# Kernel tuning notes

Hardware: AMD Instinct MI355X
Metric: run time of the kernel (lower is better)

Reference implementation:

```python
import jax, jax.numpy as jnp
import numpy as np

B, T, DM = 2, 2048, 2048
HQ, HKV, D = 16, 4, 128
MULT = 0.08838834764831845  # attn_output_multiplier = 1/sqrt(key_size)
ROPE_BASE = 10000.0


def rotate_half(x):
    x1, x2 = jnp.split(x, 2, axis=-1)
    return jnp.concatenate((-x2, x1), axis=-1)


def rope_tables(seq_len, dim, dtype):
    inv_freq = 1.0 / (ROPE_BASE ** (jnp.arange(0, dim, 2, dtype=jnp.float32) / dim))
    t = jnp.arange(seq_len, dtype=jnp.float32)
    freqs = jnp.outer(t, inv_freq)              # [T, D/2]
    emb = jnp.concatenate((freqs, freqs), axis=-1)  # [T, D]
    cos = jnp.cos(emb)[None, :, None, :].astype(dtype)  # [1, T, 1, D]
    sin = jnp.sin(emb)[None, :, None, :].astype(dtype)
    return cos, sin


def setup_inputs() -> dict:
    key = jax.random.key(0)
    ks = jax.random.split(key, 5)
    s = 1.0 / np.sqrt(DM)
    x = jax.random.normal(ks[0], (B, T, DM), dtype=jnp.float32)
    Wq = jax.random.normal(ks[1], (DM, HQ * D), dtype=jnp.float32) * s
    Wk = jax.random.normal(ks[2], (DM, HKV * D), dtype=jnp.float32) * s
    Wv = jax.random.normal(ks[3], (DM, HKV * D), dtype=jnp.float32) * s
    Wo = jax.random.normal(ks[4], (HQ * D, DM), dtype=jnp.float32) * s
    mask = jnp.tril(jnp.ones((T, T), dtype=bool))[None, None]  # [1,1,T,T] causal
    return {"x": x, "mask": mask, "Wq": Wq, "Wk": Wk, "Wv": Wv, "Wo": Wo}


def reference(x, mask, Wq, Wk, Wv, Wo):
    Bx, Tx, _ = x.shape
    q = (x @ Wq).reshape(Bx, Tx, HQ, D)
    k = (x @ Wk).reshape(Bx, Tx, HKV, D)
    v = (x @ Wv).reshape(Bx, Tx, HKV, D)
    cos, sin = rope_tables(Tx, D, x.dtype)
    q = q * cos + rotate_half(q) * sin
    k = k * cos + rotate_half(k) * sin
    n_rep = HQ // HKV
    k = jnp.repeat(k, n_rep, axis=2)  # [B,T,HQ,D] (repeat_interleave)
    v = jnp.repeat(v, n_rep, axis=2)
    logits = jnp.einsum('bqhd,bkhd->bhqk', q, k) * MULT
    logits = jnp.where(mask, logits, jnp.float32(-jnp.inf))
    attn = jax.nn.softmax(logits.astype(jnp.float32), axis=-1).astype(x.dtype)
    out = jnp.einsum('bhqk,bkhd->bqhd', attn, v).reshape(Bx, Tx, HQ * D)
    return out @ Wo
```

## Files before the change

### kernel.cpp

```cpp
#include <hip/hip_runtime.h>
#include <cstdint>
#include <cstddef>

#define T_SEQ 2048
#define DMODEL 2048
#define HQ 16
#define HKV 4
#define HD 128

typedef __attribute__((ext_vector_type(4))) float f32x4;
typedef __attribute__((ext_vector_type(8))) short bf16x8;
typedef __attribute__((ext_vector_type(4))) short short4v;
typedef __attribute__((ext_vector_type(2))) short short2v;
typedef __attribute__((ext_vector_type(4))) unsigned uint4v;

__device__ __forceinline__ short f2bf(float f) {
  unsigned u = __builtin_bit_cast(unsigned, f);
  u = (u + 0x7FFFu + ((u >> 16) & 1u)) >> 16;
  return (short)u;
}
__device__ __forceinline__ float bf2f(short s) {
  unsigned u = ((unsigned)(unsigned short)s) << 16;
  return __builtin_bit_cast(float, u);
}
__device__ __forceinline__ unsigned pk_hi16(float a, float b) {
  return __builtin_amdgcn_perm(__builtin_bit_cast(unsigned, b),
                               __builtin_bit_cast(unsigned, a), 0x07060302u);
}

__device__ __forceinline__ void g2lds16(const void* g, void* l) {
  __builtin_amdgcn_global_load_lds(
      (const __attribute__((address_space(1))) void*)g,
      (__attribute__((address_space(3))) void*)l, 16, 0, 0);
}

__global__ void cvt_kernel(const float* __restrict__ src, short* __restrict__ dst, int n) {
  int idx = blockIdx.x * 256 + threadIdx.x;
  int i = idx * 4;
  if (i >= n) return;
  float4 v = *(const float4*)(src + i);
  short4v o;
  o[0] = f2bf(v.x); o[1] = f2bf(v.y); o[2] = f2bf(v.z); o[3] = f2bf(v.w);
  *(short4v*)(dst + i) = o;
}

__global__ void transpose_cvt(const float* __restrict__ src, short* __restrict__ dst, int R, int C) {
  __shared__ float tile[32][33];
  int c0 = blockIdx.x * 32, r0 = blockIdx.y * 32;
  int tx = threadIdx.x, ty = threadIdx.y;
  #pragma unroll
  for (int i = 0; i < 32; i += 8)
    tile[ty + i][tx] = src[(size_t)(r0 + ty + i) * C + c0 + tx];
  __syncthreads();
  #pragma unroll
  for (int i = 0; i < 32; i += 8)
    dst[(size_t)(c0 + ty + i) * R + r0 + tx] = f2bf(tile[tx][ty + i]);
}

template <int MODE>
__global__ __launch_bounds__(256, 2) void gemm_kernel(
    const short* __restrict__ A, const short* __restrict__ BT,
    void* __restrict__ C0, void* __restrict__ C1, void* __restrict__ C2,
    int M, int N, int K)
{
  __shared__ short As[128 * 32];
  __shared__ short Bs[128 * 32];
  const int tid = threadIdx.x;
  const int lane = tid & 63, w = tid >> 6;
  const int l15 = lane & 15, g = lane >> 4;
  const int m0 = blockIdx.y * 128, n0 = blockIdx.x * 128;
  const int wm = (w >> 1) * 64, wn = (w & 1) * 64;

  f32x4 acc[4][4] = {};

  for (int k0 = 0; k0 < K; k0 += 32) {
    __syncthreads();
    #pragma unroll
    for (int call = 0; call < 2; call++) {
      int tau = call * 256 + tid;
      int row = tau >> 2, c = tau & 3;
      int swz = (row & 3) ^ ((row >> 2) & 3);
      g2lds16(A + (size_t)(m0 + row) * K + k0 + ((c ^ swz) << 3),
              (char*)As + call * 4096 + w * 1024);
      g2lds16(BT + (size_t)(n0 + row) * K + k0 + ((c ^ swz) << 3),
              (char*)Bs + call * 4096 + w * 1024);
    }
    __syncthreads();
    bf16x8 af[4], bfr[4];
    #pragma unroll
    for (int mi = 0; mi < 4; mi++) {
      int row = wm + mi * 16 + l15;
      int ch = g ^ ((row & 3) ^ ((row >> 2) & 3));
      af[mi] = *(const bf16x8*)(As + row * 32 + ch * 8);
    }
    #pragma unroll
    for (int ni = 0; ni < 4; ni++) {
      int row = wn + ni * 16 + l15;
      int ch = g ^ ((row & 3) ^ ((row >> 2) & 3));
      bfr[ni] = *(const bf16x8*)(Bs + row * 32 + ch * 8);
    }
    #pragma unroll
    for (int mi = 0; mi < 4; mi++)
      #pragma unroll
      for (int ni = 0; ni < 4; ni++)
        acc[mi][ni] = __builtin_amdgcn_mfma_f32_16x16x32_bf16(af[mi], bfr[ni], acc[mi][ni], 0, 0, 0);
  }

  if (MODE == 1) {
    float* C = (float*)C0;
    #pragma unroll
    for (int mi = 0; mi < 4; mi++)
      #pragma unroll
      for (int r = 0; r < 4; r++) {
        int m = m0 + wm + mi * 16 + g * 4 + r;
        #pragma unroll
        for (int ni = 0; ni < 4; ni++)
          C[(size_t)m * N + n0 + wn + ni * 16 + l15] = acc[mi][ni][r];
      }
  } else {
    short* Cb; int ldc, nc;
    if (MODE == 0) { Cb = (short*)C0; ldc = N; nc = n0; }
    else {
      if (n0 < 2048)      { Cb = (short*)C0; ldc = 2048; nc = n0; }
      else if (n0 < 2560) { Cb = (short*)C1; ldc = 512;  nc = n0 - 2048; }
      else                { Cb = (short*)C2; ldc = 512;  nc = n0 - 2560; }
    }
    #pragma unroll
    for (int mi = 0; mi < 4; mi++)
      #pragma unroll
      for (int r = 0; r < 4; r++) {
        int m = m0 + wm + mi * 16 + g * 4 + r;
        #pragma unroll
        for (int ni = 0; ni < 4; ni++)
          Cb[(size_t)m * ldc + nc + wn + ni * 16 + l15] = f2bf(acc[mi][ni][r]);
      }
  }
}

__global__ void rope_kernel(short* __restrict__ buf, int NH, float scale, int npairs) {
  int idx = blockIdx.x * 256 + threadIdx.x;
  if (idx >= npairs) return;
  int i = idx & 63;
  int th = idx >> 6;
  int t = (th / NH) % T_SEQ;
  size_t base = (size_t)th * 128;
  float invf = exp2f(-(float)i * 0.20762050593046014f);
  float theta = (float)t * invf;
  float sn, cs;
  sincosf(theta, &sn, &cs);
  float a = bf2f(buf[base + i]);
  float b = bf2f(buf[base + 64 + i]);
  buf[base + i]      = f2bf((a * cs - b * sn) * scale);
  buf[base + 64 + i] = f2bf((b * cs + a * sn) * scale);
}

__global__ __launch_bounds__(512, 4) void attn_kernel(
    const short* __restrict__ qg, const short* __restrict__ kg,
    const short* __restrict__ vg, short* __restrict__ og)
{
  __shared__ short Ks[2][64 * 128];
  __shared__ short Vt[128 * 64];
  const int tid = threadIdx.x;
  const int lane = tid & 63, w = tid >> 6;
  const int l15 = lane & 15, g = lane >> 4;
  const int b = blockIdx.z;
  const int qti = b ? (15 - (int)blockIdx.x) : (int)blockIdx.x;
  const int qt0 = qti * 128;
  const int h = blockIdx.y, hk = h >> 2;
  const int qw0 = qt0 + w * 16;

  bf16x8 qf[4];
  {
    size_t t = (size_t)b * T_SEQ + qw0 + l15;
    const short* qp = qg + (t * HQ + h) * HD;
    #pragma unroll
    for (int ks = 0; ks < 4; ks++)
      qf[ks] = *(const bf16x8*)(qp + ks * 32 + g * 8);
  }

  f32x4 of[8] = {};
  float m2 = -INFINITY;
  float ls = 0.f;

  const short* kbase = kg + ((size_t)b * T_SEQ * HKV + hk) * HD;
  const short* vbase = vg + ((size_t)b * T_SEQ * HKV + hk) * HD;

  const int kv2 = (tid & 31) * 2;
  const int d8s = (tid >> 5) * 8;
  const int p0 = (kv2 >> 5) * 32 + ((kv2 & 15) >> 2) * 8 + ((kv2 >> 4) & 1) * 4 + (kv2 & 3);
  const int nt = (qt0 + 128) >> 6;

  bf16x8 vr[2];

  auto stageK = [&](int t, int nb) {
    #pragma unroll
    for (int call = 0; call < 2; call++) {
      int tau = call * 512 + tid;
      int kv = tau >> 4, c = tau & 15;
      g2lds16(kbase + (size_t)(t * 64 + kv) * (HKV * HD) + ((c ^ (kv & 7)) << 3),
              (char*)Ks[nb] + call * 8192 + w * 1024);
    }
  };
  auto loadV = [&](int t) {
    const short* vp = vbase + (size_t)(t * 64 + kv2) * (HKV * HD) + d8s;
    vr[0] = *(const bf16x8*)(vp);
    vr[1] = *(const bf16x8*)(vp + HKV * HD);
  };
  auto writeV = [&]() {
    #pragma unroll
    for (int e = 0; e < 8; e++) {
      int row = d8s + e;
      int addr = row * 64 + (((p0 >> 3) ^ e) << 3) + (p0 & 7);
      short2v t2; t2[0] = vr[0][e]; t2[1] = vr[1][e];
      *(short2v*)(&Vt[addr]) = t2;
    }
  };

  stageK(0, 0);
  loadV(0);
  __syncthreads();
  writeV();
  __syncthreads();

  int cur = 0;
  for (int t = 0; t < nt; t++) {
    const int kv0 = t * 64;
    const bool haveNext = (t + 1 < nt);
    if (haveNext) { loadV(t + 1); stageK(t + 1, cur ^ 1); }

    if (kv0 <= qw0 + 15) {
      const short* Kc = Ks[cur];
      f32x4 sacc[4] = {};
      __builtin_amdgcn_s_setprio(1);
      #pragma unroll
      for (int ks = 0; ks < 4; ks++) {
        bf16x8 kf[4];
        #pragma unroll
        for (int kt = 0; kt < 4; kt++) {
          int row = kt * 16 + l15;
          int ch = (ks * 4 + g) ^ (row & 7);
          kf[kt] = *(const bf16x8*)(Kc + row * 128 + ch * 8);
        }
        #pragma unroll
        for (int kt = 0; kt < 4; kt++)
          sacc[kt] = __builtin_amdgcn_mfma_f32_16x16x32_bf16(kf[kt], qf[ks], sacc[kt], 0, 0, 0);
      }
      __builtin_amdgcn_s_setprio(0);
      const bool needmask = (kv0 + 63) > qw0;
      const int qpos = qw0 + l15;
      float vmax = -INFINITY;
      #pragma unroll
      for (int kt = 0; kt < 4; kt++)
        #pragma unroll
        for (int r = 0; r < 4; r++) {
          int kvpos = kv0 + kt * 16 + g * 4 + r;
          float sv = sacc[kt][r];
          if (needmask && kvpos > qpos) sv = -INFINITY;
          sacc[kt][r] = sv;
          vmax = fmaxf(vmax, sv);
        }
      vmax = fmaxf(vmax, __shfl_xor(vmax, 16));
      vmax = fmaxf(vmax, __shfl_xor(vmax, 32));
      if (!__all(vmax <= m2 + 8.0f)) {
        float mnew = fmaxf(m2, vmax);
        float resc = exp2f(m2 - mnew);
        m2 = mnew;
        ls *= resc;
        #pragma unroll
        for (int dc = 0; dc < 8; dc++) of[dc] *= resc;
      }
      float lsum = 0.f;
      #pragma unroll
      for (int kt = 0; kt < 4; kt++)
        #pragma unroll
        for (int r = 0; r < 4; r++) {
          float p = exp2f(sacc[kt][r] - m2);
          sacc[kt][r] = p;
          lsum += p;
        }
      lsum += __shfl_xor(lsum, 16);
      lsum += __shfl_xor(lsum, 32);
      ls += lsum;
      bf16x8 pb[2];
      #pragma unroll
      for (int ktw = 0; ktw < 2; ktw++) {
        uint4v pw;
        pw[0] = pk_hi16(sacc[2 * ktw][0], sacc[2 * ktw][1]);
        pw[1] = pk_hi16(sacc[2 * ktw][2], sacc[2 * ktw][3]);
        pw[2] = pk_hi16(sacc[2 * ktw + 1][0], sacc[2 * ktw + 1][1]);
        pw[3] = pk_hi16(sacc[2 * ktw + 1][2], sacc[2 * ktw + 1][3]);
        pb[ktw] = __builtin_bit_cast(bf16x8, pw);
      }
      __builtin_amdgcn_s_setprio(1);
      #pragma unroll
      for (int ktw = 0; ktw < 2; ktw++)
        #pragma unroll
        for (int dc = 0; dc < 8; dc++) {
          int row = dc * 16 + l15;
          bf16x8 vf = *(const bf16x8*)(&Vt[row * 64 + ((ktw * 32 + g * 8) ^ ((l15 & 7) << 3))]);
          of[dc] = __builtin_amdgcn_mfma_f32_16x16x32_bf16(vf, pb[ktw], of[dc], 0, 0, 0);
        }
      __builtin_amdgcn_s_setprio(0);
    }

    __syncthreads();
    if (haveNext) writeV();
    __syncthreads();
    cur ^= 1;
  }

  {
    float inv = 1.0f / ls;
    size_t t = (size_t)b * T_SEQ + qw0 + l15;
    short* op = og + (t * HQ + h) * HD;
    #pragma unroll
    for (int dc = 0; dc < 8; dc++) {
      short4v o;
      #pragma unroll
      for (int r = 0; r < 4; r++) o[r] = f2bf(of[dc][r] * inv);
      *(short4v*)(op + dc * 16 + g * 4) = o;
    }
  }
}

extern "C" void kernel_launch(void* const* d_in, const int* in_sizes, int n_in,
                              void* d_out, int out_size, void* d_ws, size_t ws_size,
                              hipStream_t stream) {
  (void)in_sizes; (void)n_in; (void)out_size; (void)ws_size;
  const float* x  = (const float*)d_in[0];
  const float* Wq = (const float*)d_in[2];
  const float* Wk = (const float*)d_in[3];
  const float* Wv = (const float*)d_in[4];
  const float* Wo = (const float*)d_in[5];

  char* ws = (char*)d_ws;
  short* xb   = (short*)(ws);
  short* wall = (short*)(ws + 16777216);
  short* wkT  = wall + (size_t)2048 * 2048;
  short* wvT  = wall + (size_t)2560 * 2048;
  short* woT  = (short*)(ws + 29360128);
  short* qb   = (short*)(ws + 37748736);
  short* kb   = (short*)(ws + 54525952);
  short* vb   = (short*)(ws + 58720256);
  short* ab   = (short*)(ws + 62914560);

  const float MULT = 0.08838834764831845f;
  const float LOG2E = 1.4426950408889634f;
  const float QSCALE = MULT * LOG2E;

  dim3 tb(32, 8);
  cvt_kernel<<<8192, 256, 0, stream>>>(x, xb, 8388608);
  transpose_cvt<<<dim3(64, 64), tb, 0, stream>>>(Wq, wall, 2048, 2048);
  transpose_cvt<<<dim3(16, 64), tb, 0, stream>>>(Wk, wkT, 2048, 512);
  transpose_cvt<<<dim3(16, 64), tb, 0, stream>>>(Wv, wvT, 2048, 512);
  transpose_cvt<<<dim3(64, 64), tb, 0, stream>>>(Wo, woT, 2048, 2048);

  gemm_kernel<2><<<dim3(24, 32), 256, 0, stream>>>(xb, wall, qb, kb, vb, 4096, 3072, 2048);

  rope_kernel<<<16384, 256, 0, stream>>>(qb, HQ, QSCALE, 4194304);
  rope_kernel<<<4096, 256, 0, stream>>>(kb, HKV, 1.0f, 1048576);

  attn_kernel<<<dim3(16, 16, 2), 512, 0, stream>>>(qb, kb, vb, ab);

  gemm_kernel<1><<<dim3(16, 32), 256, 0, stream>>>(ab, woT, d_out, nullptr, nullptr, 4096, 2048, 2048);
}
```

Measured before the change: 231.6 us.

## Split KV range for long causal query tiles and merge with combine kernel

The last eight query tiles (the most work under the causal mask) are split into two blocks that each take alternate KV tiles. Each block writes a normalized partial output plus its max and sum, and a new combine kernel merges the two halves. This balances per-block work and raises the block count from 512 to 768. It costs an extra launch and extra partial-output traffic, and it reuses the xb and weight workspace regions after the QKV gemm. It also defers the row-sum shuffle reduction to the end of the loop and raises the launch-bounds occupancy hint to 6.

```diff
diff --git a/kernel.cpp b/kernel.cpp
--- a/kernel.cpp
+++ b/kernel.cpp
@@ -154,9 +154,10 @@
   buf[base + 64 + i] = f2bf((b * cs + a * sn) * scale);
 }
 
-__global__ __launch_bounds__(512, 4) void attn_kernel(
+__global__ __launch_bounds__(512, 6) void attn_kernel(
     const short* __restrict__ qg, const short* __restrict__ kg,
-    const short* __restrict__ vg, short* __restrict__ og)
+    const short* __restrict__ vg, short* __restrict__ og,
+    short* __restrict__ pOn, float2* __restrict__ ml)
 {
   __shared__ short Ks[2][64 * 128];
   __shared__ short Vt[128 * 64];
@@ -164,7 +165,11 @@
   const int lane = tid & 63, w = tid >> 6;
   const int l15 = lane & 15, g = lane >> 4;
   const int b = blockIdx.z;
-  const int qti = b ? (15 - (int)blockIdx.x) : (int)blockIdx.x;
+  const int bx = blockIdx.x;
+  const bool split = bx < 16;
+  const int qti = split ? (8 + (bx >> 1)) : (bx - 16);
+  const int hf = split ? (bx & 1) : 0;
+  const int tstep = split ? 2 : 1;
   const int qt0 = qti * 128;
   const int h = blockIdx.y, hk = h >> 2;
   const int qw0 = qt0 + w * 16;
@@ -188,7 +193,7 @@
   const int kv2 = (tid & 31) * 2;
   const int d8s = (tid >> 5) * 8;
   const int p0 = (kv2 >> 5) * 32 + ((kv2 & 15) >> 2) * 8 + ((kv2 >> 4) & 1) * 4 + (kv2 & 3);
-  const int nt = (qt0 + 128) >> 6;
+  const int ntAll = 2 * qti + 2;
 
   bf16x8 vr[2];
 
@@ -216,20 +221,21 @@
     }
   };
 
-  stageK(0, 0);
-  loadV(0);
+  stageK(hf, 0);
+  loadV(hf);
   __syncthreads();
   writeV();
   __syncthreads();
 
-  int cur = 0;
-  for (int t = 0; t < nt; t++) {
+  int buf = 0;
+  for (int t = hf; t < ntAll; t += tstep) {
     const int kv0 = t * 64;
-    const bool haveNext = (t + 1 < nt);
-    if (haveNext) { loadV(t + 1); stageK(t + 1, cur ^ 1); }
+    const int tn = t + tstep;
+    const bool haveNext = (tn < ntAll);
+    if (haveNext) { loadV(tn); stageK(tn, buf ^ 1); }
 
     if (kv0 <= qw0 + 15) {
-      const short* Kc = Ks[cur];
+      const short* Kc = Ks[buf];
       f32x4 sacc[4] = {};
       __builtin_amdgcn_s_setprio(1);
       #pragma unroll
@@ -269,18 +275,14 @@
         #pragma unroll
         for (int dc = 0; dc < 8; dc++) of[dc] *= resc;
       }
-      float lsum = 0.f;
       #pragma unroll
       for (int kt = 0; kt < 4; kt++)
         #pragma unroll
         for (int r = 0; r < 4; r++) {
           float p = exp2f(sacc[kt][r] - m2);
           sacc[kt][r] = p;
-          lsum += p;
+          ls += p;
         }
-      lsum += __shfl_xor(lsum, 16);
-      lsum += __shfl_xor(lsum, 32);
-      ls += lsum;
       bf16x8 pb[2];
       #pragma unroll
       for (int ktw = 0; ktw < 2; ktw++) {
@@ -306,11 +308,13 @@
     __syncthreads();
     if (haveNext) writeV();
     __syncthreads();
-    cur ^= 1;
+    buf ^= 1;
   }
 
-  {
-    float inv = 1.0f / ls;
+  ls += __shfl_xor(ls, 16);
+  ls += __shfl_xor(ls, 32);
+  float inv = 1.0f / ls;
+  if (!split) {
     size_t t = (size_t)b * T_SEQ + qw0 + l15;
     short* op = og + (t * HQ + h) * HD;
     #pragma unroll
@@ -320,7 +324,44 @@
       for (int r = 0; r < 4; r++) o[r] = f2bf(of[dc][r] * inv);
       *(short4v*)(op + dc * 16 + g * 4) = o;
     }
+  } else {
+    size_t row = ((size_t)((b * 16 + h) * 2 + hf)) * 1024 + (qw0 - 1024) + l15;
+    short* op = pOn + row * 128;
+    #pragma unroll
+    for (int dc = 0; dc < 8; dc++) {
+      short4v o;
+      #pragma unroll
+      for (int r = 0; r < 4; r++) o[r] = f2bf(of[dc][r] * inv);
+      *(short4v*)(op + dc * 16 + g * 4) = o;
+    }
+    if (g == 0) {
+      float2 st; st.x = m2; st.y = ls;
+      ml[row] = st;
+    }
   }
+}
+
+__global__ void combine_kernel(const short* __restrict__ pOn, const float2* __restrict__ ml,
+                               short* __restrict__ ab) {
+  int idx = blockIdx.x * 256 + threadIdx.x;
+  int d4 = (idx & 31) * 4;
+  int r = idx >> 5;
+  int q = r & 1023, bh = r >> 10;
+  size_t row0 = ((size_t)bh * 2) * 1024 + q;
+  size_t row1 = row0 + 1024;
+  float2 s0 = ml[row0], s1 = ml[row1];
+  float M = fmaxf(s0.x, s1.x);
+  float w0 = s0.y * exp2f(s0.x - M);
+  float w1 = s1.y * exp2f(s1.x - M);
+  float inv = 1.0f / (w0 + w1);
+  w0 *= inv; w1 *= inv;
+  short4v a = *(const short4v*)(pOn + row0 * 128 + d4);
+  short4v c = *(const short4v*)(pOn + row1 * 128 + d4);
+  short4v o;
+  #pragma unroll
+  for (int j = 0; j < 4; j++) o[j] = f2bf(w0 * bf2f(a[j]) + w1 * bf2f(c[j]));
+  int bb = bh >> 4, hh = bh & 15;
+  *(short4v*)(ab + ((size_t)(bb * T_SEQ + 1024 + q) * 16 + hh) * 128 + d4) = o;
 }
 
 extern "C" void kernel_launch(void* const* d_in, const int* in_sizes, int n_in,
@@ -334,15 +375,17 @@
   const float* Wo = (const float*)d_in[5];
 
   char* ws = (char*)d_ws;
-  short* xb   = (short*)(ws);
-  short* wall = (short*)(ws + 16777216);
-  short* wkT  = wall + (size_t)2048 * 2048;
-  short* wvT  = wall + (size_t)2560 * 2048;
-  short* woT  = (short*)(ws + 29360128);
-  short* qb   = (short*)(ws + 37748736);
-  short* kb   = (short*)(ws + 54525952);
-  short* vb   = (short*)(ws + 58720256);
-  short* ab   = (short*)(ws + 62914560);
+  short*  xb   = (short*)(ws);
+  short*  wall = (short*)(ws + 16777216);
+  short*  wkT  = wall + (size_t)2048 * 2048;
+  short*  wvT  = wall + (size_t)2560 * 2048;
+  short*  pOn  = (short*)(ws);
+  float2* ml   = (float2*)(ws + 16777216);
+  short*  woT  = (short*)(ws + 29360128);
+  short*  qb   = (short*)(ws + 37748736);
+  short*  kb   = (short*)(ws + 54525952);
+  short*  vb   = (short*)(ws + 58720256);
+  short*  ab   = (short*)(ws + 62914560);
 
   const float MULT = 0.08838834764831845f;
   const float LOG2E = 1.4426950408889634f;
@@ -360,7 +403,8 @@
   rope_kernel<<<16384, 256, 0, stream>>>(qb, HQ, QSCALE, 4194304);
   rope_kernel<<<4096, 256, 0, stream>>>(kb, HKV, 1.0f, 1048576);
 
-  attn_kernel<<<dim3(16, 16, 2), 512, 0, stream>>>(qb, kb, vb, ab);
+  attn_kernel<<<dim3(24, 16, 2), 512, 0, stream>>>(qb, kb, vb, ab, pOn, ml);
+  combine_kernel<<<4096, 256, 0, stream>>>(pOn, ml, ab);
 
   gemm_kernel<1><<<dim3(16, 32), 256, 0, stream>>>(ab, woT, d_out, nullptr, nullptr, 4096, 2048, 2048);
 }
```

After: 392.3 us. +69.4%, slower.
